# Kernel optimization log

Measured on AMD Instinct MI355X. Metric: run time of the kernel, lower is better.

The kernel has to match this reference:

```python
import jax, jax.numpy as jnp
import numpy as np

N, E, IN, OUT, R, B = 20000, 640000, 256, 800, 8, 8


def setup_inputs() -> dict:
    key = jax.random.key(0)
    k0, k1, k2, k3, k4, k5 = jax.random.split(key, 6)
    x = jax.random.normal(k0, (N, IN), dtype=jnp.float32)
    edge_index = jax.random.randint(k1, (2, E), 0, N, dtype=jnp.int32)
    edge_type = jax.random.randint(k2, (E,), 0, R, dtype=jnp.int32)
    # basis-decomposed relation weights: W_r = sum_b att[r,b] * bases[b]
    bases = jax.random.normal(k3, (B, IN, OUT), dtype=jnp.float32) * 0.05
    att = jax.random.normal(k4, (R, B), dtype=jnp.float32) * 0.3
    root = jax.random.normal(k5, (IN, OUT), dtype=jnp.float32) * 0.05
    bias = jnp.zeros((OUT,), dtype=jnp.float32)
    return {"x": x, "edge_index": edge_index, "edge_type": edge_type,
            "bases": bases, "att": att, "root": root, "bias": bias}


def reference(x, edge_index, edge_type, bases, att, root, bias):
    # RGCNConv (basis decomposition, scatter-add aggregation):
    #   out[v] = sum_{(u->v, r) in edges} x[u] @ W_r  +  x[v] @ root  +  bias
    # Efficient form: first segment-sum x[src] per (dst, relation), then one
    # dense contraction with the R relation weights (math-identical for add-aggr).
    n, in_dim = x.shape
    r, b = att.shape
    W = jnp.einsum('rb,bio->rio', att, bases)          # [R, IN, OUT]
    src, dst = edge_index[0], edge_index[1]
    seg = dst.astype(jnp.int32) * r + edge_type.astype(jnp.int32)
    # per-(node, relation) sums of source features: [N*R, IN] -> [N, R, IN]
    s = jax.ops.segment_sum(x[src], seg, num_segments=n * r).reshape(n, r, in_dim)
    out = jnp.einsum('nri,rio->no', s, W) + x @ root + bias
    return out
```

## Files before the change

kernel.cpp:

```cpp
#include <hip/hip_runtime.h>


#define N_NODES 20000
#define N_EDGES 640000
#define IN_DIM  256
#define OUT_DIM 800
#define NREL    8
#define NSEG    160000
#define KS      2048
#define KTOT    2304
#define NPAD    1024
#define NB      625

#define BM 128
#define BN 256
#define BK 64
#define NKT (KTOT / BK)
#define MT  157
#define NT  4
#define NWG (MT * NT)
#define LBUF 49152

#define XCAST_B (N_NODES * 64 / 256)
#define WCAT_B  ((KTOT / 8) * 4)
#define INIT_NWG (NB + XCAST_B + WCAT_B)

typedef float f32x4_t __attribute__((ext_vector_type(4)));
typedef short short8_t __attribute__((ext_vector_type(8)));

__device__ __forceinline__ unsigned short f2bf(float f) {
  unsigned u = __float_as_uint(f);
  u += 0x7fffu + ((u >> 16) & 1u);
  return (unsigned short)(u >> 16);
}

__device__ __forceinline__ float bflo(unsigned w) { return __uint_as_float(w << 16); }
__device__ __forceinline__ float bfhi(unsigned w) { return __uint_as_float(w & 0xffff0000u); }

__device__ __forceinline__ void gload16(const void* g, void* l) {
  __builtin_amdgcn_global_load_lds(
      (const __attribute__((address_space(1))) void*)g,
      (__attribute__((address_space(3))) void*)l, 16, 0, 0);
}

__global__ void init_kernel(const float* __restrict__ x,
                            const float* __restrict__ bases,
                            const float* __restrict__ att,
                            const float* __restrict__ root,
                            int* __restrict__ cnt,
                            unsigned short* __restrict__ abf,
                            unsigned short* __restrict__ wcatT) {
  const int b = blockIdx.x;
  const int t = threadIdx.x;
  if (b < NB) {
    cnt[b * 256 + t] = 0;
  } else if (b < NB + XCAST_B) {
    const int id = (b - NB) * 256 + t;
    const int row = id >> 6, lane = id & 63;
    const float4 v = ((const float4*)x)[(size_t)row * 64 + lane];
    union { unsigned short u[4]; uint2 q; } pk;
    pk.u[0] = f2bf(v.x); pk.u[1] = f2bf(v.y);
    pk.u[2] = f2bf(v.z); pk.u[3] = f2bf(v.w);
    *(uint2*)(abf + (size_t)row * KTOT + KS + lane * 4) = pk.q;
  } else {
    const int rem = b - NB - XCAST_B;
    const int kc = rem >> 2, ng = rem & 3;
    const int k0 = kc * 8;
    const int n  = ng * 256 + t;
    union { unsigned short u[8]; uint4 q; } pk;
    if (n >= OUT_DIM) {
      pk.q = make_uint4(0u, 0u, 0u, 0u);
    } else if (k0 < KS) {
      const int r = k0 >> 8, i0 = k0 & 255;
      float av[8];
      #pragma unroll
      for (int bb = 0; bb < 8; ++bb) av[bb] = att[r * 8 + bb];
      #pragma unroll
      for (int j = 0; j < 8; ++j) {
        float v = 0.f;
        #pragma unroll
        for (int bb = 0; bb < 8; ++bb)
          v += av[bb] * bases[((size_t)bb * IN_DIM + i0 + j) * OUT_DIM + n];
        pk.u[j] = f2bf(v);
      }
    } else {
      #pragma unroll
      for (int j = 0; j < 8; ++j)
        pk.u[j] = f2bf(root[(size_t)(k0 - KS + j) * OUT_DIM + n]);
    }
    *(uint4*)(wcatT + (size_t)n * KTOT + k0) = pk.q;
  }
}


__global__ void hist_kernel(const int* __restrict__ ei, const int* __restrict__ et,
                            int* __restrict__ cnt) {
  const int e = blockIdx.x * 256 + threadIdx.x;
  const int seg = ei[N_EDGES + e] * NREL + et[e];
  atomicAdd(&cnt[seg], 1);
}

__global__ void scan_reduce_kernel(const int* __restrict__ cnt, int* __restrict__ bsum) {
  __shared__ int sm[256];
  const int t = threadIdx.x;
  sm[t] = cnt[blockIdx.x * 256 + t];
  __syncthreads();
  for (int s = 128; s > 0; s >>= 1) {
    if (t < s) sm[t] += sm[t + s];
    __syncthreads();
  }
  if (t == 0) bsum[blockIdx.x] = sm[0];
}

__global__ void scan_bsum_kernel(int* __restrict__ bsum) {
  __shared__ int sm[1024];
  const int t = threadIdx.x;
  const int v = (t < NB) ? bsum[t] : 0;
  sm[t] = v;
  __syncthreads();
  for (int s = 1; s < 1024; s <<= 1) {
    const int a = (t >= s) ? sm[t - s] : 0;
    __syncthreads();
    sm[t] += a;
    __syncthreads();
  }
  if (t < NB) bsum[t] = sm[t] - v;
}

__global__ void scan_final_kernel(const int* __restrict__ cnt, const int* __restrict__ bsum,
                                  int* __restrict__ off, int* __restrict__ cur) {
  __shared__ int sm[256];
  const int t = threadIdx.x;
  const int g = blockIdx.x * 256 + t;
  const int v = cnt[g];
  sm[t] = v;
  __syncthreads();
  for (int s = 1; s < 256; s <<= 1) {
    const int a = (t >= s) ? sm[t - s] : 0;
    __syncthreads();
    sm[t] += a;
    __syncthreads();
  }
  const int ex = sm[t] - v + bsum[blockIdx.x];
  off[g] = ex;
  cur[g] = ex;
}

__global__ void reorder_kernel(const int* __restrict__ ei, const int* __restrict__ et,
                               int* __restrict__ cur, int* __restrict__ sorted_src) {
  const int e = blockIdx.x * 256 + threadIdx.x;
  const int seg = ei[N_EDGES + e] * NREL + et[e];
  const int pos = atomicAdd(&cur[seg], 1);
  sorted_src[pos] = ei[e];
}

__global__ void aggregate_kernel(const int* __restrict__ cnt, const int* __restrict__ off,
                                 const int* __restrict__ sorted_src,
                                 unsigned short* __restrict__ abf) {
  const int seg = __builtin_amdgcn_readfirstlane(blockIdx.x * 4 + (threadIdx.x >> 6));
  const int l = threadIdx.x & 63;
  const int half = l >> 5;
  const int sl = l & 31;
  const int ne = cnt[seg];
  const int o  = off[seg];
  float a0 = 0.f, a1 = 0.f, a2 = 0.f, a3 = 0.f;
  float a4 = 0.f, a5 = 0.f, a6 = 0.f, a7 = 0.f;
  int j = 0;
  for (; j + 2 <= ne; j += 2) {
    const int s = sorted_src[o + j + half];
    const uint4 u = *(const uint4*)(abf + (size_t)s * KTOT + KS + sl * 8);
    a0 += bflo(u.x); a1 += bfhi(u.x); a2 += bflo(u.y); a3 += bfhi(u.y);
    a4 += bflo(u.z); a5 += bfhi(u.z); a6 += bflo(u.w); a7 += bfhi(u.w);
  }
  if (j < ne && half == 0) {
    const int s = sorted_src[o + j];
    const uint4 u = *(const uint4*)(abf + (size_t)s * KTOT + KS + sl * 8);
    a0 += bflo(u.x); a1 += bfhi(u.x); a2 += bflo(u.y); a3 += bfhi(u.y);
    a4 += bflo(u.z); a5 += bfhi(u.z); a6 += bflo(u.w); a7 += bfhi(u.w);
  }
  a0 += __shfl_xor(a0, 32); a1 += __shfl_xor(a1, 32);
  a2 += __shfl_xor(a2, 32); a3 += __shfl_xor(a3, 32);
  a4 += __shfl_xor(a4, 32); a5 += __shfl_xor(a5, 32);
  a6 += __shfl_xor(a6, 32); a7 += __shfl_xor(a7, 32);
  if (half == 0) {
    const int node = seg >> 3, r = seg & 7;
    union { unsigned short u[8]; uint4 q; } pk;
    pk.u[0] = f2bf(a0); pk.u[1] = f2bf(a1); pk.u[2] = f2bf(a2); pk.u[3] = f2bf(a3);
    pk.u[4] = f2bf(a4); pk.u[5] = f2bf(a5); pk.u[6] = f2bf(a6); pk.u[7] = f2bf(a7);
    *(uint4*)(abf + (size_t)node * KTOT + r * IN_DIM + sl * 8) = pk.q;
  }
}

__global__ __launch_bounds__(512) void gemm_kernel(
    const unsigned short* __restrict__ abf,
    const unsigned short* __restrict__ wcatT,
    const float* __restrict__ bias, float* __restrict__ out) {
  __shared__ __align__(16) char lds[3 * LBUF];

  const int lin = blockIdx.x;
  const int q8 = NWG >> 3, r8 = NWG & 7;
  const int xcd = lin & 7, idx = lin >> 3;
  const int wg = (xcd < r8 ? xcd * (q8 + 1) : r8 * (q8 + 1) + (xcd - r8) * q8) + idx;
  const int row0 = (wg / NT) * BM;
  const int col0 = (wg % NT) * BN;

  const int tid = threadIdx.x;
  const int w = tid >> 6, l = tid & 63;
  const int wm = w >> 2, wn = w & 3;
  const int la = l & 15, lg = l >> 4;
  const int l3 = l >> 3;
  const int sch = (l & 7) ^ l3;

  const unsigned short* gA[2];
  const unsigned short* gB[4];
  #pragma unroll
  for (int i = 0; i < 2; ++i) {
    int ga = row0 + i * 64 + w * 8 + l3;
    ga = (ga < N_NODES) ? ga : (N_NODES - 1);
    gA[i] = abf + (size_t)ga * KTOT + sch * 8;
  }
  #pragma unroll
  for (int i = 0; i < 4; ++i)
    gB[i] = wcatT + (size_t)(col0 + i * 64 + w * 8 + l3) * KTOT + sch * 8;

  f32x4_t acc[4][4];
  #pragma unroll
  for (int i = 0; i < 4; ++i)
    #pragma unroll
    for (int j = 0; j < 4; ++j)
      acc[i][j] = (f32x4_t)(0.0f);

  auto stage_all = [&](int buf, int kt) {
    char* pA = lds + buf * LBUF + w * 1024;
    char* pB = pA + 16384;
    const int ko = kt * BK;
    gload16(gA[0] + ko, pA);
    gload16(gA[1] + ko, pA + 8192);
    gload16(gB[0] + ko, pB);
    gload16(gB[1] + ko, pB + 8192);
    gload16(gB[2] + ko, pB + 16384);
    gload16(gB[3] + ko, pB + 24576);
  };

  stage_all(0, 0);
  stage_all(1, 1);

  for (int kt = 0; kt < NKT; ++kt) {
    const int cbuf = kt % 3;
    const int pbuf = (kt + 2) % 3;
    const bool pf = (kt + 2) < NKT;
    const int pko = (kt + 2) * BK;
    const char* Ab = lds + cbuf * LBUF;
    const char* Bb = Ab + 16384;
    char* pA = lds + pbuf * LBUF + w * 1024;
    char* pB = pA + 16384;

    if (kt + 1 < NKT) { asm volatile("s_waitcnt vmcnt(6)" ::: "memory"); }
    else              { asm volatile("s_waitcnt vmcnt(0)" ::: "memory"); }
    __builtin_amdgcn_sched_barrier(0);
    __builtin_amdgcn_s_barrier();

    short8_t af0, af1, bf0, bf1, bf2, bf3;

    {
      const int r0 = wm * 64 + la,       r1 = wm * 64 + 16 + la;
      af0 = *(const short8_t*)(Ab + r0 * 128 + ((lg << 4) ^ ((r0 & 7) << 4)));
      af1 = *(const short8_t*)(Ab + r1 * 128 + ((lg << 4) ^ ((r1 & 7) << 4)));
      #pragma unroll
      for (int nf = 0; nf < 4; ++nf) {
        const int rr = wn * 64 + nf * 16 + la;
        const short8_t v = *(const short8_t*)(Bb + rr * 128 + ((lg << 4) ^ ((rr & 7) << 4)));
        if (nf == 0) bf0 = v; else if (nf == 1) bf1 = v; else if (nf == 2) bf2 = v; else bf3 = v;
      }
      if (pf) { gload16(gA[0] + pko, pA); gload16(gA[1] + pko, pA + 8192); }
      __builtin_amdgcn_s_barrier();
      asm volatile("s_waitcnt lgkmcnt(0)" ::: "memory");
      __builtin_amdgcn_sched_barrier(0);
      __builtin_amdgcn_s_setprio(1);
      acc[0][0] = __builtin_amdgcn_mfma_f32_16x16x32_bf16(af0, bf0, acc[0][0], 0, 0, 0);
      acc[0][1] = __builtin_amdgcn_mfma_f32_16x16x32_bf16(af0, bf1, acc[0][1], 0, 0, 0);
      acc[0][2] = __builtin_amdgcn_mfma_f32_16x16x32_bf16(af0, bf2, acc[0][2], 0, 0, 0);
      acc[0][3] = __builtin_amdgcn_mfma_f32_16x16x32_bf16(af0, bf3, acc[0][3], 0, 0, 0);
      acc[1][0] = __builtin_amdgcn_mfma_f32_16x16x32_bf16(af1, bf0, acc[1][0], 0, 0, 0);
      acc[1][1] = __builtin_amdgcn_mfma_f32_16x16x32_bf16(af1, bf1, acc[1][1], 0, 0, 0);
      acc[1][2] = __builtin_amdgcn_mfma_f32_16x16x32_bf16(af1, bf2, acc[1][2], 0, 0, 0);
      acc[1][3] = __builtin_amdgcn_mfma_f32_16x16x32_bf16(af1, bf3, acc[1][3], 0, 0, 0);
      __builtin_amdgcn_s_setprio(0);
      __builtin_amdgcn_s_barrier();
    }
    {
      const int r0 = wm * 64 + 32 + la,  r1 = wm * 64 + 48 + la;
      af0 = *(const short8_t*)(Ab + r0 * 128 + ((lg << 4) ^ ((r0 & 7) << 4)));
      af1 = *(const short8_t*)(Ab + r1 * 128 + ((lg << 4) ^ ((r1 & 7) << 4)));
      if (pf) { gload16(gB[0] + pko, pB); gload16(gB[1] + pko, pB + 8192); }
      __builtin_amdgcn_s_barrier();
      asm volatile("s_waitcnt lgkmcnt(0)" ::: "memory");
      __builtin_amdgcn_sched_barrier(0);
      __builtin_amdgcn_s_setprio(1);
      acc[2][0] = __builtin_amdgcn_mfma_f32_16x16x32_bf16(af0, bf0, acc[2][0], 0, 0, 0);
      acc[2][1] = __builtin_amdgcn_mfma_f32_16x16x32_bf16(af0, bf1, acc[2][1], 0, 0, 0);
      acc[2][2] = __builtin_amdgcn_mfma_f32_16x16x32_bf16(af0, bf2, acc[2][2], 0, 0, 0);
      acc[2][3] = __builtin_amdgcn_mfma_f32_16x16x32_bf16(af0, bf3, acc[2][3], 0, 0, 0);
      acc[3][0] = __builtin_amdgcn_mfma_f32_16x16x32_bf16(af1, bf0, acc[3][0], 0, 0, 0);
      acc[3][1] = __builtin_amdgcn_mfma_f32_16x16x32_bf16(af1, bf1, acc[3][1], 0, 0, 0);
      acc[3][2] = __builtin_amdgcn_mfma_f32_16x16x32_bf16(af1, bf2, acc[3][2], 0, 0, 0);
      acc[3][3] = __builtin_amdgcn_mfma_f32_16x16x32_bf16(af1, bf3, acc[3][3], 0, 0, 0);
      __builtin_amdgcn_s_setprio(0);
      __builtin_amdgcn_s_barrier();
    }
    {
      const int r0 = wm * 64 + la,       r1 = wm * 64 + 16 + la;
      af0 = *(const short8_t*)(Ab + r0 * 128 + (((4 + lg) << 4) ^ ((r0 & 7) << 4)));
      af1 = *(const short8_t*)(Ab + r1 * 128 + (((4 + lg) << 4) ^ ((r1 & 7) << 4)));
      #pragma unroll
      for (int nf = 0; nf < 4; ++nf) {
        const int rr = wn * 64 + nf * 16 + la;
        const short8_t v = *(const short8_t*)(Bb + rr * 128 + (((4 + lg) << 4) ^ ((rr & 7) << 4)));
        if (nf == 0) bf0 = v; else if (nf == 1) bf1 = v; else if (nf == 2) bf2 = v; else bf3 = v;
      }
      if (pf) { gload16(gB[2] + pko, pB + 16384); gload16(gB[3] + pko, pB + 24576); }
      __builtin_amdgcn_s_barrier();
      asm volatile("s_waitcnt lgkmcnt(0)" ::: "memory");
      __builtin_amdgcn_sched_barrier(0);
      __builtin_amdgcn_s_setprio(1);
      acc[0][0] = __builtin_amdgcn_mfma_f32_16x16x32_bf16(af0, bf0, acc[0][0], 0, 0, 0);
      acc[0][1] = __builtin_amdgcn_mfma_f32_16x16x32_bf16(af0, bf1, acc[0][1], 0, 0, 0);
      acc[0][2] = __builtin_amdgcn_mfma_f32_16x16x32_bf16(af0, bf2, acc[0][2], 0, 0, 0);
      acc[0][3] = __builtin_amdgcn_mfma_f32_16x16x32_bf16(af0, bf3, acc[0][3], 0, 0, 0);
      acc[1][0] = __builtin_amdgcn_mfma_f32_16x16x32_bf16(af1, bf0, acc[1][0], 0, 0, 0);
      acc[1][1] = __builtin_amdgcn_mfma_f32_16x16x32_bf16(af1, bf1, acc[1][1], 0, 0, 0);
      acc[1][2] = __builtin_amdgcn_mfma_f32_16x16x32_bf16(af1, bf2, acc[1][2], 0, 0, 0);
      acc[1][3] = __builtin_amdgcn_mfma_f32_16x16x32_bf16(af1, bf3, acc[1][3], 0, 0, 0);
      __builtin_amdgcn_s_setprio(0);
      __builtin_amdgcn_s_barrier();
    }
    {
      const int r0 = wm * 64 + 32 + la,  r1 = wm * 64 + 48 + la;
      af0 = *(const short8_t*)(Ab + r0 * 128 + (((4 + lg) << 4) ^ ((r0 & 7) << 4)));
      af1 = *(const short8_t*)(Ab + r1 * 128 + (((4 + lg) << 4) ^ ((r1 & 7) << 4)));
      __builtin_amdgcn_s_barrier();
      asm volatile("s_waitcnt lgkmcnt(0)" ::: "memory");
      __builtin_amdgcn_sched_barrier(0);
      __builtin_amdgcn_s_setprio(1);
      acc[2][0] = __builtin_amdgcn_mfma_f32_16x16x32_bf16(af0, bf0, acc[2][0], 0, 0, 0);
      acc[2][1] = __builtin_amdgcn_mfma_f32_16x16x32_bf16(af0, bf1, acc[2][1], 0, 0, 0);
      acc[2][2] = __builtin_amdgcn_mfma_f32_16x16x32_bf16(af0, bf2, acc[2][2], 0, 0, 0);
      acc[2][3] = __builtin_amdgcn_mfma_f32_16x16x32_bf16(af0, bf3, acc[2][3], 0, 0, 0);
      acc[3][0] = __builtin_amdgcn_mfma_f32_16x16x32_bf16(af1, bf0, acc[3][0], 0, 0, 0);
      acc[3][1] = __builtin_amdgcn_mfma_f32_16x16x32_bf16(af1, bf1, acc[3][1], 0, 0, 0);
      acc[3][2] = __builtin_amdgcn_mfma_f32_16x16x32_bf16(af1, bf2, acc[3][2], 0, 0, 0);
      acc[3][3] = __builtin_amdgcn_mfma_f32_16x16x32_bf16(af1, bf3, acc[3][3], 0, 0, 0);
      __builtin_amdgcn_s_setprio(0);
      __builtin_amdgcn_s_barrier();
    }
  }

  #pragma unroll
  for (int nf = 0; nf < 4; ++nf) {
    const int gcol = col0 + wn * 64 + nf * 16 + la;
    if (gcol < OUT_DIM) {
      const float bv = bias[gcol];
      #pragma unroll
      for (int f = 0; f < 4; ++f) {
        const int gr0 = row0 + wm * 64 + f * 16 + lg * 4;
        #pragma unroll
        for (int j = 0; j < 4; ++j) {
          const int gr = gr0 + j;
          if (gr < N_NODES)
            out[(size_t)gr * OUT_DIM + gcol] = acc[f][nf][j] + bv;
        }
      }
    }
  }
}

extern "C" void kernel_launch(void* const* d_in, const int* in_sizes, int n_in,
                              void* d_out, int out_size, void* d_ws, size_t ws_size,
                              hipStream_t stream) {
  const float* x     = (const float*)d_in[0];
  const int*   ei    = (const int*)d_in[1];
  const int*   et    = (const int*)d_in[2];
  const float* bases = (const float*)d_in[3];
  const float* att   = (const float*)d_in[4];
  const float* root  = (const float*)d_in[5];
  const float* bias  = (const float*)d_in[6];
  float* out = (float*)d_out;

  char* p = (char*)d_ws;
  unsigned short* abf   = (unsigned short*)p;  p += (size_t)N_NODES * KTOT * 2;
  unsigned short* wcatT = (unsigned short*)p;  p += (size_t)NPAD * KTOT * 2;
  int* cnt        = (int*)p;                   p += (size_t)NSEG * 4;
  int* off        = (int*)p;                   p += (size_t)NSEG * 4;
  int* cur        = (int*)p;                   p += (size_t)NSEG * 4;
  int* sorted_src = (int*)p;                   p += (size_t)N_EDGES * 4;
  int* bsum       = (int*)p;                   p += 4096;

  init_kernel<<<INIT_NWG, 256, 0, stream>>>(x, bases, att, root, cnt, abf, wcatT);
  hist_kernel<<<N_EDGES / 256, 256, 0, stream>>>(ei, et, cnt);
  scan_reduce_kernel<<<NB, 256, 0, stream>>>(cnt, bsum);
  scan_bsum_kernel<<<1, 1024, 0, stream>>>(bsum);
  scan_final_kernel<<<NB, 256, 0, stream>>>(cnt, bsum, off, cur);
  reorder_kernel<<<N_EDGES / 256, 256, 0, stream>>>(ei, et, cur, sorted_src);
  aggregate_kernel<<<NSEG / 4, 256, 0, stream>>>(cnt, off, sorted_src, abf);
  gemm_kernel<<<NWG, 512, 0, stream>>>(abf, wcatT, bias, out);
}
```

Baseline: 257.8 us.

## Retile GEMM to 256x160 blocks so OUT_DIM divides evenly without padding

The GEMM tile changes from 128x256 to 256x160, so the 800 output columns split into exactly 5 column tiles instead of 4 padded ones. Waves are rearranged into 4x2 with 5 B fragments each, the LDS staging plan and waitcnt counts are reworked, and the wcatT init skips writing padded columns. This removes the wasted MFMA work and loads on the padded columns and raises arithmetic intensity per block, in exchange for more LDS per buffer, more accumulator registers, and fewer workgroups (395 vs 628), which may underfill the GPU.

```diff
diff --git a/kernel.cpp b/kernel.cpp
--- a/kernel.cpp
+++ b/kernel.cpp
@@ -12,14 +12,15 @@
 #define NPAD    1024
 #define NB      625
 
-#define BM 128
-#define BN 256
+#define BM 256
+#define BN 160
 #define BK 64
 #define NKT (KTOT / BK)
-#define MT  157
-#define NT  4
+#define MT  79
+#define NT  5
 #define NWG (MT * NT)
-#define LBUF 49152
+#define ABYTES 32768
+#define LBUF 53248
 
 #define XCAST_B (N_NODES * 64 / 256)
 #define WCAT_B  ((KTOT / 8) * 4)
@@ -67,10 +68,9 @@
     const int kc = rem >> 2, ng = rem & 3;
     const int k0 = kc * 8;
     const int n  = ng * 256 + t;
+    if (n >= OUT_DIM) return;
     union { unsigned short u[8]; uint4 q; } pk;
-    if (n >= OUT_DIM) {
-      pk.q = make_uint4(0u, 0u, 0u, 0u);
-    } else if (k0 < KS) {
+    if (k0 < KS) {
       const int r = k0 >> 8, i0 = k0 & 255;
       float av[8];
       #pragma unroll
@@ -206,40 +206,41 @@
 
   const int tid = threadIdx.x;
   const int w = tid >> 6, l = tid & 63;
-  const int wm = w >> 2, wn = w & 3;
+  const int wm = w >> 1, wn = w & 1;
   const int la = l & 15, lg = l >> 4;
   const int l3 = l >> 3;
   const int sch = (l & 7) ^ l3;
 
-  const unsigned short* gA[2];
-  const unsigned short* gB[4];
+  const unsigned short* gA[4];
   #pragma unroll
-  for (int i = 0; i < 2; ++i) {
+  for (int i = 0; i < 4; ++i) {
     int ga = row0 + i * 64 + w * 8 + l3;
     ga = (ga < N_NODES) ? ga : (N_NODES - 1);
     gA[i] = abf + (size_t)ga * KTOT + sch * 8;
   }
-  #pragma unroll
-  for (int i = 0; i < 4; ++i)
-    gB[i] = wcatT + (size_t)(col0 + i * 64 + w * 8 + l3) * KTOT + sch * 8;
-
-  f32x4_t acc[4][4];
+  const int b2row = (w < 4) ? (128 + w * 8 + l3) : ((w - 4) * 8 + l3);
+  const unsigned short* gB0 = wcatT + (size_t)(col0 + w * 8 + l3) * KTOT + sch * 8;
+  const unsigned short* gB1 = wcatT + (size_t)(col0 + 64 + w * 8 + l3) * KTOT + sch * 8;
+  const unsigned short* gB2 = wcatT + (size_t)(col0 + b2row) * KTOT + sch * 8;
+  const int dB2 = (w < 4) ? (ABYTES + 16384 + w * 1024) : (ABYTES + (w - 4) * 1024);
+
+  f32x4_t acc[4][5];
   #pragma unroll
   for (int i = 0; i < 4; ++i)
     #pragma unroll
-    for (int j = 0; j < 4; ++j)
+    for (int j = 0; j < 5; ++j)
       acc[i][j] = (f32x4_t)(0.0f);
 
   auto stage_all = [&](int buf, int kt) {
-    char* pA = lds + buf * LBUF + w * 1024;
-    char* pB = pA + 16384;
+    char* base = lds + buf * LBUF;
     const int ko = kt * BK;
-    gload16(gA[0] + ko, pA);
-    gload16(gA[1] + ko, pA + 8192);
-    gload16(gB[0] + ko, pB);
-    gload16(gB[1] + ko, pB + 8192);
-    gload16(gB[2] + ko, pB + 16384);
-    gload16(gB[3] + ko, pB + 24576);
+    gload16(gA[0] + ko, base + w * 1024);
+    gload16(gA[1] + ko, base + 8192 + w * 1024);
+    gload16(gA[2] + ko, base + 16384 + w * 1024);
+    gload16(gA[3] + ko, base + 24576 + w * 1024);
+    gload16(gB0 + ko, base + ABYTES + w * 1024);
+    gload16(gB1 + ko, base + ABYTES + 8192 + w * 1024);
+    gload16(gB2 + ko, base + dB2);
   };
 
   stage_all(0, 0);
@@ -251,124 +252,115 @@
     const bool pf = (kt + 2) < NKT;
     const int pko = (kt + 2) * BK;
     const char* Ab = lds + cbuf * LBUF;
-    const char* Bb = Ab + 16384;
-    char* pA = lds + pbuf * LBUF + w * 1024;
-    char* pB = pA + 16384;
-
-    if (kt + 1 < NKT) { asm volatile("s_waitcnt vmcnt(6)" ::: "memory"); }
+    const char* Bb = Ab + ABYTES;
+    char* pbase = lds + pbuf * LBUF;
+
+    if (kt + 1 < NKT) { asm volatile("s_waitcnt vmcnt(7)" ::: "memory"); }
     else              { asm volatile("s_waitcnt vmcnt(0)" ::: "memory"); }
     __builtin_amdgcn_sched_barrier(0);
     __builtin_amdgcn_s_barrier();
 
-    short8_t af0, af1, bf0, bf1, bf2, bf3;
+    short8_t af0, af1, bfv[5];
 
     {
-      const int r0 = wm * 64 + la,       r1 = wm * 64 + 16 + la;
+      const int r0 = wm * 64 + la, r1 = wm * 64 + 16 + la;
       af0 = *(const short8_t*)(Ab + r0 * 128 + ((lg << 4) ^ ((r0 & 7) << 4)));
       af1 = *(const short8_t*)(Ab + r1 * 128 + ((lg << 4) ^ ((r1 & 7) << 4)));
       #pragma unroll
-      for (int nf = 0; nf < 4; ++nf) {
-        const int rr = wn * 64 + nf * 16 + la;
-        const short8_t v = *(const short8_t*)(Bb + rr * 128 + ((lg << 4) ^ ((rr & 7) << 4)));
-        if (nf == 0) bf0 = v; else if (nf == 1) bf1 = v; else if (nf == 2) bf2 = v; else bf3 = v;
+      for (int nf = 0; nf < 5; ++nf) {
+        const int rr = wn * 80 + nf * 16 + la;
+        bfv[nf] = *(const short8_t*)(Bb + rr * 128 + ((lg << 4) ^ ((rr & 7) << 4)));
       }
-      if (pf) { gload16(gA[0] + pko, pA); gload16(gA[1] + pko, pA + 8192); }
+      if (pf) { gload16(gA[0] + pko, pbase + w * 1024);
+                gload16(gA[1] + pko, pbase + 8192 + w * 1024); }
       __builtin_amdgcn_s_barrier();
       asm volatile("s_waitcnt lgkmcnt(0)" ::: "memory");
       __builtin_amdgcn_sched_barrier(0);
       __builtin_amdgcn_s_setprio(1);
-      acc[0][0] = __builtin_amdgcn_mfma_f32_16x16x32_bf16(af0, bf0, acc[0][0], 0, 0, 0);
-      acc[0][1] = __builtin_amdgcn_mfma_f32_16x16x32_bf16(af0, bf1, acc[0][1], 0, 0, 0);
-      acc[0][2] = __builtin_amdgcn_mfma_f32_16x16x32_bf16(af0, bf2, acc[0][2], 0, 0, 0);
-      acc[0][3] = __builtin_amdgcn_mfma_f32_16x16x32_bf16(af0, bf3, acc[0][3], 0, 0, 0);
-      acc[1][0] = __builtin_amdgcn_mfma_f32_16x16x32_bf16(af1, bf0, acc[1][0], 0, 0, 0);
-      acc[1][1] = __builtin_amdgcn_mfma_f32_16x16x32_bf16(af1, bf1, acc[1][1], 0, 0, 0);
-      acc[1][2] = __builtin_amdgcn_mfma_f32_16x16x32_bf16(af1, bf2, acc[1][2], 0, 0, 0);
-      acc[1][3] = __builtin_amdgcn_mfma_f32_16x16x32_bf16(af1, bf3, acc[1][3], 0, 0, 0);
+      #pragma unroll
+      for (int nf = 0; nf < 5; ++nf)
+        acc[0][nf] = __builtin_amdgcn_mfma_f32_16x16x32_bf16(af0, bfv[nf], acc[0][nf], 0, 0, 0);
+      #pragma unroll
+      for (int nf = 0; nf < 5; ++nf)
+        acc[1][nf] = __builtin_amdgcn_mfma_f32_16x16x32_bf16(af1, bfv[nf], acc[1][nf], 0, 0, 0);
       __builtin_amdgcn_s_setprio(0);
       __builtin_amdgcn_s_barrier();
     }
     {
-      const int r0 = wm * 64 + 32 + la,  r1 = wm * 64 + 48 + la;
+      const int r0 = wm * 64 + 32 + la, r1 = wm * 64 + 48 + la;
       af0 = *(const short8_t*)(Ab + r0 * 128 + ((lg << 4) ^ ((r0 & 7) << 4)));
       af1 = *(const short8_t*)(Ab + r1 * 128 + ((lg << 4) ^ ((r1 & 7) << 4)));
-      if (pf) { gload16(gB[0] + pko, pB); gload16(gB[1] + pko, pB + 8192); }
+      if (pf) { gload16(gA[2] + pko, pbase + 16384 + w * 1024);
+                gload16(gA[3] + pko, pbase + 24576 + w * 1024); }
       __builtin_amdgcn_s_barrier();
       asm volatile("s_waitcnt lgkmcnt(0)" ::: "memory");
       __builtin_amdgcn_sched_barrier(0);
       __builtin_amdgcn_s_setprio(1);
-      acc[2][0] = __builtin_amdgcn_mfma_f32_16x16x32_bf16(af0, bf0, acc[2][0], 0, 0, 0);
-      acc[2][1] = __builtin_amdgcn_mfma_f32_16x16x32_bf16(af0, bf1, acc[2][1], 0, 0, 0);
-      acc[2][2] = __builtin_amdgcn_mfma_f32_16x16x32_bf16(af0, bf2, acc[2][2], 0, 0, 0);
-      acc[2][3] = __builtin_amdgcn_mfma_f32_16x16x32_bf16(af0, bf3, acc[2][3], 0, 0, 0);
-      acc[3][0] = __builtin_amdgcn_mfma_f32_16x16x32_bf16(af1, bf0, acc[3][0], 0, 0, 0);
-      acc[3][1] = __builtin_amdgcn_mfma_f32_16x16x32_bf16(af1, bf1, acc[3][1], 0, 0, 0);
-      acc[3][2] = __builtin_amdgcn_mfma_f32_16x16x32_bf16(af1, bf2, acc[3][2], 0, 0, 0);
-      acc[3][3] = __builtin_amdgcn_mfma_f32_16x16x32_bf16(af1, bf3, acc[3][3], 0, 0, 0);
+      #pragma unroll
+      for (int nf = 0; nf < 5; ++nf)
+        acc[2][nf] = __builtin_amdgcn_mfma_f32_16x16x32_bf16(af0, bfv[nf], acc[2][nf], 0, 0, 0);
+      #pragma unroll
+      for (int nf = 0; nf < 5; ++nf)
+        acc[3][nf] = __builtin_amdgcn_mfma_f32_16x16x32_bf16(af1, bfv[nf], acc[3][nf], 0, 0, 0);
       __builtin_amdgcn_s_setprio(0);
       __builtin_amdgcn_s_barrier();
     }
     {
-      const int r0 = wm * 64 + la,       r1 = wm * 64 + 16 + la;
+      const int r0 = wm * 64 + la, r1 = wm * 64 + 16 + la;
       af0 = *(const short8_t*)(Ab + r0 * 128 + (((4 + lg) << 4) ^ ((r0 & 7) << 4)));
       af1 = *(const short8_t*)(Ab + r1 * 128 + (((4 + lg) << 4) ^ ((r1 & 7) << 4)));
       #pragma unroll
-      for (int nf = 0; nf < 4; ++nf) {
-        const int rr = wn * 64 + nf * 16 + la;
-        const short8_t v = *(const short8_t*)(Bb + rr * 128 + (((4 + lg) << 4) ^ ((rr & 7) << 4)));
-        if (nf == 0) bf0 = v; else if (nf == 1) bf1 = v; else if (nf == 2) bf2 = v; else bf3 = v;
+      for (int nf = 0; nf < 5; ++nf) {
+        const int rr = wn * 80 + nf * 16 + la;
+        bfv[nf] = *(const short8_t*)(Bb + rr * 128 + (((4 + lg) << 4) ^ ((rr & 7) << 4)));
       }
-      if (pf) { gload16(gB[2] + pko, pB + 16384); gload16(gB[3] + pko, pB + 24576); }
+      if (pf) { gload16(gB0 + pko, pbase + ABYTES + w * 1024);
+                gload16(gB1 + pko, pbase + ABYTES + 8192 + w * 1024); }
       __builtin_amdgcn_s_barrier();
       asm volatile("s_waitcnt lgkmcnt(0)" ::: "memory");
       __builtin_amdgcn_sched_barrier(0);
       __builtin_amdgcn_s_setprio(1);
-      acc[0][0] = __builtin_amdgcn_mfma_f32_16x16x32_bf16(af0, bf0, acc[0][0], 0, 0, 0);
-      acc[0][1] = __builtin_amdgcn_mfma_f32_16x16x32_bf16(af0, bf1, acc[0][1], 0, 0, 0);
-      acc[0][2] = __builtin_amdgcn_mfma_f32_16x16x32_bf16(af0, bf2, acc[0][2], 0, 0, 0);
-      acc[0][3] = __builtin_amdgcn_mfma_f32_16x16x32_bf16(af0, bf3, acc[0][3], 0, 0, 0);
-      acc[1][0] = __builtin_amdgcn_mfma_f32_16x16x32_bf16(af1, bf0, acc[1][0], 0, 0, 0);
-      acc[1][1] = __builtin_amdgcn_mfma_f32_16x16x32_bf16(af1, bf1, acc[1][1], 0, 0, 0);
-      acc[1][2] = __builtin_amdgcn_mfma_f32_16x16x32_bf16(af1, bf2, acc[1][2], 0, 0, 0);
-      acc[1][3] = __builtin_amdgcn_mfma_f32_16x16x32_bf16(af1, bf3, acc[1][3], 0, 0, 0);
+      #pragma unroll
+      for (int nf = 0; nf < 5; ++nf)
+        acc[0][nf] = __builtin_amdgcn_mfma_f32_16x16x32_bf16(af0, bfv[nf], acc[0][nf], 0, 0, 0);
+      #pragma unroll
+      for (int nf = 0; nf < 5; ++nf)
+        acc[1][nf] = __builtin_amdgcn_mfma_f32_16x16x32_bf16(af1, bfv[nf], acc[1][nf], 0, 0, 0);
       __builtin_amdgcn_s_setprio(0);
       __builtin_amdgcn_s_barrier();
     }
     {
-      const int r0 = wm * 64 + 32 + la,  r1 = wm * 64 + 48 + la;
+      const int r0 = wm * 64 + 32 + la, r1 = wm * 64 + 48 + la;
       af0 = *(const short8_t*)(Ab + r0 * 128 + (((4 + lg) << 4) ^ ((r0 & 7) << 4)));
       af1 = *(const short8_t*)(Ab + r1 * 128 + (((4 + lg) << 4) ^ ((r1 & 7) << 4)));
+      if (pf) { gload16(gB2 + pko, pbase + dB2); }
       __builtin_amdgcn_s_barrier();
       asm volatile("s_waitcnt lgkmcnt(0)" ::: "memory");
       __builtin_amdgcn_sched_barrier(0);
       __builtin_amdgcn_s_setprio(1);
-      acc[2][0] = __builtin_amdgcn_mfma_f32_16x16x32_bf16(af0, bf0, acc[2][0], 0, 0, 0);
-      acc[2][1] = __builtin_amdgcn_mfma_f32_16x16x32_bf16(af0, bf1, acc[2][1], 0, 0, 0);
-      acc[2][2] = __builtin_amdgcn_mfma_f32_16x16x32_bf16(af0, bf2, acc[2][2], 0, 0, 0);
-      acc[2][3] = __builtin_amdgcn_mfma_f32_16x16x32_bf16(af0, bf3, acc[2][3], 0, 0, 0);
-      acc[3][0] = __builtin_amdgcn_mfma_f32_16x16x32_bf16(af1, bf0, acc[3][0], 0, 0, 0);
-      acc[3][1] = __builtin_amdgcn_mfma_f32_16x16x32_bf16(af1, bf1, acc[3][1], 0, 0, 0);
-      acc[3][2] = __builtin_amdgcn_mfma_f32_16x16x32_bf16(af1, bf2, acc[3][2], 0, 0, 0);
-      acc[3][3] = __builtin_amdgcn_mfma_f32_16x16x32_bf16(af1, bf3, acc[3][3], 0, 0, 0);
+      #pragma unroll
+      for (int nf = 0; nf < 5; ++nf)
+        acc[2][nf] = __builtin_amdgcn_mfma_f32_16x16x32_bf16(af0, bfv[nf], acc[2][nf], 0, 0, 0);
+      #pragma unroll
+      for (int nf = 0; nf < 5; ++nf)
+        acc[3][nf] = __builtin_amdgcn_mfma_f32_16x16x32_bf16(af1, bfv[nf], acc[3][nf], 0, 0, 0);
       __builtin_amdgcn_s_setprio(0);
       __builtin_amdgcn_s_barrier();
     }
   }
 
   #pragma unroll
-  for (int nf = 0; nf < 4; ++nf) {
-    const int gcol = col0 + wn * 64 + nf * 16 + la;
-    if (gcol < OUT_DIM) {
-      const float bv = bias[gcol];
-      #pragma unroll
-      for (int f = 0; f < 4; ++f) {
-        const int gr0 = row0 + wm * 64 + f * 16 + lg * 4;
-        #pragma unroll
-        for (int j = 0; j < 4; ++j) {
-          const int gr = gr0 + j;
-          if (gr < N_NODES)
-            out[(size_t)gr * OUT_DIM + gcol] = acc[f][nf][j] + bv;
-        }
+  for (int nf = 0; nf < 5; ++nf) {
+    const int gcol = col0 + wn * 80 + nf * 16 + la;
+    const float bv = bias[gcol];
+    #pragma unroll
+    for (int f = 0; f < 4; ++f) {
+      const int gr0 = row0 + wm * 64 + f * 16 + lg * 4;
+      #pragma unroll
+      for (int j = 0; j < 4; ++j) {
+        const int gr = gr0 + j;
+        if (gr < N_NODES)
+          out[(size_t)gr * OUT_DIM + gcol] = acc[f][nf][j] + bv;
       }
     }
   }
```

Result: faster. 241.8 us (-6.2%).
